# Kernel optimization log

Measured on AMD Instinct MI355X. Metric: run time of the kernel, lower is better.

## Reference

```python
import jax, jax.numpy as jnp
import numpy as np

N_NODES = 200000
N_EDGES = 6400000
IN_CH, HID, OUT_CH = 14, 16, 2


def gcn_conv(x, W, b, src, dst, n_nodes):
    """GCNConv with self-loops and symmetric normalization (PyG defaults).

    out[i] = sum_{j->i} d[i]^-1/2 d[j]^-1/2 (xW)[j] + d[i]^-1 (xW)[i] + b,
    where d = degree(A + I) computed on the target index.
    """
    h = x @ W  # [N, F_out]
    ones = jnp.ones((src.shape[0],), dtype=x.dtype)
    deg = jax.ops.segment_sum(ones, dst, num_segments=n_nodes) + 1.0  # +1 self-loop
    dinv = jax.lax.rsqrt(deg)  # [N]
    norm = dinv[src] * dinv[dst]  # [E]
    msg = h[src] * norm[:, None]  # [E, F_out] -- dominant memory traffic
    agg = jax.ops.segment_sum(msg, dst, num_segments=n_nodes)
    self_loop = h * (dinv * dinv)[:, None]
    return agg + self_loop + b


def setup_inputs() -> dict:
    key = jax.random.key(0)
    k1, k2, k3, k4, k5 = jax.random.split(key, 5)
    x = jax.random.normal(k1, (N_NODES, IN_CH), dtype=jnp.float32)
    edge_index = jax.random.randint(k2, (2, N_EDGES), 0, N_NODES, dtype=jnp.int64)
    edge_attr = jax.random.normal(k3, (N_EDGES, 1), dtype=jnp.float32)  # unused by GCNConv
    s = 1.0 / np.sqrt(IN_CH)
    W1 = jax.random.uniform(k4, (IN_CH, HID), jnp.float32, -s, s)
    b1 = jnp.zeros((HID,), jnp.float32)
    s2 = 1.0 / np.sqrt(HID)
    W2 = jax.random.uniform(k5, (HID, OUT_CH), jnp.float32, -s2, s2)
    b2 = jnp.zeros((OUT_CH,), jnp.float32)
    return {"x": x, "edge_index": edge_index, "edge_attr": edge_attr,
            "W1": W1, "b1": b1, "W2": W2, "b2": b2}


def reference(x, edge_index, edge_attr, W1, b1, W2, b2):
    src, dst = edge_index[0], edge_index[1]
    n = x.shape[0]
    h = jax.nn.relu(gcn_conv(x, W1, b1, src, dst, n))
    # F.dropout(training=self.training) is identity in eval mode
    out = gcn_conv(h, W2, b2, src, dst, n)
    return out
```

## Files before the change

kernel.cpp:

```cpp
#include <hip/hip_runtime.h>
#include <hip/hip_fp16.h>


constexpr int NN = 200000;
constexpr int NE = 6400000;
constexpr int IC = 14;
constexpr int HC = 16;
constexpr int OC = 2;

constexpr int NBK = 392;
constexpr int NSUB = 8;
constexpr int SCAP = 2816;
constexpr int NSEG = NSUB * NBK;
constexpr int CCAP = NSUB * SCAP;
constexpr int SPT = (SCAP + 1023) / 1024;
constexpr int TILE = 5120;
constexpr int BTH = 512;
constexpr int IPT = TILE / BTH;
constexpr int IPT2 = IPT / 2;
constexpr int NTILE = NE / TILE;
constexpr int OVFCAP = 65536;
constexpr int NM = NN / 32;
constexpr int GSTR = 16;

typedef unsigned long long ull;
typedef float f4v __attribute__((ext_vector_type(4)));

__device__ __forceinline__ int phase_of(unsigned src) {
    return src >= 100000u ? (src >= 150000u ? 3 : 2) : (src >= 50000u ? 1 : 0);
}

__device__ __forceinline__ int xcc_id() {
    int x;
    asm volatile("s_getreg_b32 %0, hwreg(HW_REG_XCC_ID)" : "=s"(x));
    return x & 7;
}

__device__ __forceinline__ void acc8(float* av, uint4 u) {
    float2 f0 = __half22float2(*(__half2*)&u.x);
    float2 f1 = __half22float2(*(__half2*)&u.y);
    float2 f2 = __half22float2(*(__half2*)&u.z);
    float2 f3 = __half22float2(*(__half2*)&u.w);
    av[0] += f0.x; av[1] += f0.y; av[2] += f1.x; av[3] += f1.y;
    av[4] += f2.x; av[5] += f2.y; av[6] += f3.x; av[7] += f3.y;
}

__global__ void k_init(int* __restrict__ gcur, const void* __restrict__ ei,
                       int* __restrict__ flag) {
    int i = blockIdx.x * blockDim.x + threadIdx.x;
    if (i < NSEG) gcur[i * GSTR] = i * SCAP;
    else if (i <= NSEG + 4) gcur[i * GSTR] = 0;
    if (i == 500) {
        const ull* p = (const ull*)ei;
        ull acc = 0ULL;
        for (int k = 0; k < 64; ++k) acc |= (p[k] >> 32);
        *flag = (acc == 0ULL) ? 1 : 0;
    }
}

__global__ __launch_bounds__(BTH, 6) void k_binA(const void* __restrict__ ei,
                                                 const int* __restrict__ flag,
                                                 int* __restrict__ gcur,
                                                 unsigned* __restrict__ binned,
                                                 ull* __restrict__ ovf) {
    __shared__ int hist[NBK];
    __shared__ int lofs[NBK];
    __shared__ int gofs[NBK];
    __shared__ int wsum[BTH / 64];
    __shared__ unsigned stage[TILE];

    int t = threadIdx.x;
    int fl = *flag;
    int tile0 = blockIdx.x * TILE;
    int segbase = xcc_id() * NBK;

    if (t < NBK) hist[t] = 0;
    __syncthreads();

    int dbuf[IPT], sbuf[IPT];
    const int* pw = (const int*)ei;
    if (fl) {
#pragma unroll
        for (int k = 0; k < IPT2; ++k) {
            int e = tile0 + k * (2 * BTH) + 2 * t;
            ulonglong2 dd = *(const ulonglong2*)((const long long*)ei + NE + e);
            ulonglong2 ss = *(const ulonglong2*)((const long long*)ei + e);
            dbuf[2 * k] = (int)dd.x;
            dbuf[2 * k + 1] = (int)dd.y;
            sbuf[2 * k] = (int)ss.x;
            sbuf[2 * k + 1] = (int)ss.y;
        }
    } else {
#pragma unroll
        for (int k = 0; k < IPT2; ++k) {
            int e = tile0 + k * (2 * BTH) + 2 * t;
            uint2 dd = *(const uint2*)(pw + NE + e);
            uint2 ss = *(const uint2*)(pw + e);
            dbuf[2 * k] = (int)dd.x;
            dbuf[2 * k + 1] = (int)dd.y;
            sbuf[2 * k] = (int)ss.x;
            sbuf[2 * k + 1] = (int)ss.y;
        }
    }

    unsigned pk[IPT];
    unsigned ra[IPT];
#pragma unroll
    for (int k = 0; k < IPT; ++k) {
        int d = dbuf[k];
        int b = d >> 9;
        int r = atomicAdd(&hist[b], 1);
        pk[k] = ((unsigned)(d & 511) << 18) | (unsigned)sbuf[k];
        ra[k] = ((unsigned)r << 9) | (unsigned)b;
    }
    __syncthreads();

    int h0 = 0, h1 = 0, p = 0;
    if (t < NBK / 2) {
        h0 = hist[2 * t];
        h1 = hist[2 * t + 1];
        p = h0 + h1;
    }
    int lane = t & 63;
    int w = t >> 6;
    int incl = p;
#pragma unroll
    for (int off = 1; off < 64; off <<= 1) {
        int v = __shfl_up(incl, off, 64);
        if (lane >= off) incl += v;
    }
    if (lane == 63) wsum[w] = incl;
    __syncthreads();
    int wbase = 0;
#pragma unroll
    for (int ww = 0; ww < BTH / 64; ++ww) wbase += (ww < w) ? wsum[ww] : 0;
    int ex = wbase + incl - p;
    if (t < NBK / 2) {
        lofs[2 * t] = ex;
        lofs[2 * t + 1] = ex + h0;
    }
    if (t < NBK) gofs[t] = atomicAdd(&gcur[(segbase + t) * GSTR], hist[t]);
    __syncthreads();

#pragma unroll
    for (int k = 0; k < IPT; ++k) {
        int b = (int)(ra[k] & 511u);
        int r = (int)(ra[k] >> 9);
        stage[lofs[b] + r] = pk[k];
    }
    __syncthreads();

    for (int i = t; i < TILE; i += BTH) {
        int b = (i * 313) >> 12;
        if (b > NBK - 1) b = NBK - 1;
        while (b < NBK - 1 && lofs[b + 1] <= i) ++b;
        while (lofs[b] > i) --b;
        unsigned pack = stage[i];
        int seg = segbase + b;
        int dest = gofs[b] + (i - lofs[b]);
        if (dest < (seg + 1) * SCAP) {
            binned[dest] = pack;
        } else {
            int op = atomicAdd(&gcur[NSEG * GSTR], 1);
            if (op < OVFCAP) {
                int d = (b << 9) | (int)(pack >> 18);
                int s = (int)(pack & 0x3FFFF);
                ovf[op] = ((ull)d << 32) | (unsigned)s;
            }
        }
    }
}

__global__ __launch_bounds__(1024, 4) void k_sort(const int* __restrict__ gcur,
                                                  const unsigned* __restrict__ binned,
                                                  const ull* __restrict__ ovf,
                                                  const float* __restrict__ x,
                                                  unsigned* __restrict__ csr,
                                                  float* __restrict__ dinv,
                                                  int* __restrict__ rsg,
                                                  unsigned* __restrict__ spl,
                                                  __half* __restrict__ xph) {
    __shared__ int cnt[2048];
    __shared__ int excl[2048];
    __shared__ int wsum[16];
    __shared__ int nseg[NSUB];
    __shared__ float sdv[512];
    __shared__ unsigned stage[CCAP];
    int b = blockIdx.x;
    int t = threadIdx.x;
    cnt[t] = 0;
    cnt[t + 1024] = 0;
    if (t < NSUB) {
        int seg = t * NBK + b;
        nseg[t] = min(gcur[seg * GSTR] - seg * SCAP, SCAP);
    }
    __syncthreads();
    int nov = min(gcur[NSEG * GSTR], OVFCAP);

    unsigned srcv[NSUB * SPT];
    unsigned rkv[NSUB * SPT];
#pragma unroll
    for (int s = 0; s < NSUB; ++s) {
        int n = nseg[s];
        int sb = (s * NBK + b) * SCAP;
#pragma unroll
        for (int k = 0; k < SPT; ++k) {
            int i = k * 1024 + t;
            rkv[s * SPT + k] = 0xFFFFFFFFu;
            if (i < n) {
                unsigned pack = binned[sb + i];
                unsigned src = pack & 0x3FFFFu;
                int key = ((int)(pack >> 18) << 2) | phase_of(src);
                int r = atomicAdd(&cnt[key], 1);
                srcv[s * SPT + k] = src;
                rkv[s * SPT + k] = ((unsigned)r << 11) | (unsigned)key;
            }
        }
    }
    __syncthreads();

    int h0 = cnt[2 * t];
    int h1 = cnt[2 * t + 1];
    int p = h0 + h1;
    int lane = t & 63;
    int w = t >> 6;
    int incl = p;
#pragma unroll
    for (int off = 1; off < 64; off <<= 1) {
        int v = __shfl_up(incl, off, 64);
        if (lane >= off) incl += v;
    }
    if (lane == 63) wsum[w] = incl;
    __syncthreads();
    int wbase = 0;
#pragma unroll
    for (int ww = 0; ww < 16; ++ww) wbase += (ww < w) ? wsum[ww] : 0;
    int ex = wbase + incl - p;
    excl[2 * t] = ex;
    excl[2 * t + 1] = ex + h0;
    __syncthreads();

#pragma unroll
    for (int c = 0; c < NSUB * SPT; ++c) {
        unsigned rk = rkv[c];
        if (rk != 0xFFFFFFFFu) {
            int key = (int)(rk & 0x7FFu);
            int r = (int)(rk >> 11);
            stage[excl[key] + r] = srcv[c];
        }
    }

    if (t < 512) {
        int g = (b << 9) + t;
        if (g < NN) {
            int c0 = cnt[4 * t];
            int c1 = cnt[4 * t + 1];
            int c2 = cnt[4 * t + 2];
            int c3 = cnt[4 * t + 3];
            int extra = 0;
            for (int k = 0; k < nov; ++k) extra += ((int)(ovf[k] >> 32) == g);
            float dv = rsqrtf((float)(c0 + c1 + c2 + c3 + extra) + 1.0f);
            dinv[g] = dv;
            sdv[t] = dv;
            rsg[g] = b * CCAP + excl[4 * t];
            spl[g] = (unsigned)c0 | ((unsigned)c1 << 8) |
                     ((unsigned)c2 << 16) | ((unsigned)c3 << 24);
        }
    }
    __syncthreads();

    int total = excl[2047] + cnt[2047];
    int tot4 = (total + 3) >> 2;
    const uint4* st4 = (const uint4*)stage;
    uint4* csr4 = (uint4*)(csr + (size_t)b * CCAP);
#pragma unroll
    for (int k = 0; k < (CCAP / 4 + 1023) / 1024; ++k) {
        int i4 = k * 1024 + t;
        if (i4 < tot4) csr4[i4] = st4[i4];
    }

    {
        int n512 = t >> 1;
        int g = (b << 9) + n512;
        if (g < NN) {
            float dv = sdv[n512];
            int cb = 8 * (t & 1);
            const float* xr = x + (size_t)g * IC;
            float v[8];
#pragma unroll
            for (int c = 0; c < 8; c += 2) {
                int ch = cb + c;
                if (ch + 1 < IC) {
                    float2 xx = *(const float2*)(xr + ch);
                    v[c] = dv * xx.x;
                    v[c + 1] = dv * xx.y;
                } else {
                    v[c] = 0.0f;
                    v[c + 1] = 0.0f;
                }
            }
            __half2 p0 = __floats2half2_rn(v[0], v[1]);
            __half2 p1 = __floats2half2_rn(v[2], v[3]);
            __half2 p2 = __floats2half2_rn(v[4], v[5]);
            __half2 p3 = __floats2half2_rn(v[6], v[7]);
            uint4 pk4;
            pk4.x = *(unsigned*)&p0;
            pk4.y = *(unsigned*)&p1;
            pk4.z = *(unsigned*)&p2;
            pk4.w = *(unsigned*)&p3;
            *(uint4*)(xph + (size_t)g * 16 + cb) = pk4;
        }
    }
}

__global__ __launch_bounds__(256) void k_agg1f(const int* __restrict__ rsg,
                                               const unsigned* __restrict__ spl,
                                               const unsigned* __restrict__ csr,
                                               const __half* __restrict__ xph,
                                               const int* __restrict__ gcur,
                                               const ull* __restrict__ ovf,
                                               const float* __restrict__ dinv,
                                               const float* __restrict__ W1,
                                               const float* __restrict__ b1,
                                               const float* __restrict__ W2,
                                               const float* __restrict__ b2,
                                               float2* __restrict__ h2bp,
                                               float2* __restrict__ selfout) {
    __shared__ float sW1[IC * HC];
    __shared__ float sb1[HC];
    __shared__ float sW2[HC * OC];
    __shared__ float sb2[OC];
    __shared__ float sAgg[32][17];
    int t = threadIdx.x;
    if (t < IC * HC) sW1[t] = W1[t];
    if (t < HC) sb1[t] = b1[t];
    if (t < HC * OC) sW2[t] = W2[t];
    if (t < OC) sb2[t] = b2[t];

    int g = t >> 3;
    int h = t & 7;
    int qc = h & 1;
    int eh = h >> 1;
    int i = blockIdx.x * 32 + g;
    unsigned sp = spl[i];
    int tot = (int)(sp & 255u) + (int)((sp >> 8) & 255u) +
              (int)((sp >> 16) & 255u) + (int)(sp >> 24);
    int beg = rsg[i];
    int end = beg + tot;

    float av[8];
#pragma unroll
    for (int c = 0; c < 8; ++c) av[c] = 0.0f;
    int j = beg + eh;
    int s0 = (j < end) ? (int)csr[j] : -1;
    int s1 = (j + 4 < end) ? (int)csr[j + 4] : -1;
    while (j < end) {
        int jn = j + 8;
        int n0 = (jn < end) ? (int)csr[jn] : -1;
        int n1 = (jn + 4 < end) ? (int)csr[jn + 4] : -1;
        uint4 u0 = *(const uint4*)(xph + (size_t)s0 * 16 + 8 * qc);
        acc8(av, u0);
        if (s1 >= 0) {
            uint4 u1 = *(const uint4*)(xph + (size_t)s1 * 16 + 8 * qc);
            acc8(av, u1);
        }
        s0 = n0;
        s1 = n1;
        j = jn;
    }

    if (eh == 0) {
        uint4 us = *(const uint4*)(xph + (size_t)i * 16 + 8 * qc);
        acc8(av, us);
    }
#pragma unroll
    for (int c = 0; c < 8; ++c) av[c] += __shfl_xor(av[c], 2);
#pragma unroll
    for (int c = 0; c < 8; ++c) av[c] += __shfl_xor(av[c], 4);

    float dv = dinv[i];
    if (eh == 0) {
        int nov = min(gcur[NSEG * GSTR], OVFCAP);
        for (int k = 0; k < nov; ++k) {
            ull e = ovf[k];
            if ((int)(e >> 32) == i) {
                int s = (int)(e & 0xFFFFFFFFu);
#pragma unroll
                for (int c = 0; c < 8; ++c)
                    av[c] += __half2float(xph[(size_t)s * 16 + 8 * qc + c]);
            }
        }
#pragma unroll
        for (int c = 0; c < 8; ++c) sAgg[g][8 * qc + c] = dv * av[c];
    }
    __syncthreads();

    int l8 = t & 7;
    float o0 = 0.0f, o1 = 0.0f;
#pragma unroll
    for (int f2 = 0; f2 < 2; ++f2) {
        int f = 2 * l8 + f2;
        float a = sb1[f];
#pragma unroll
        for (int c = 0; c < IC; ++c) a = fmaf(sAgg[g][c], sW1[c * HC + f], a);
        a = fmaxf(a, 0.0f);
        o0 = fmaf(a, sW2[f * OC + 0], o0);
        o1 = fmaf(a, sW2[f * OC + 1], o1);
    }
    o0 += __shfl_xor(o0, 1);
    o1 += __shfl_xor(o1, 1);
    o0 += __shfl_xor(o0, 2);
    o1 += __shfl_xor(o1, 2);
    o0 += __shfl_xor(o0, 4);
    o1 += __shfl_xor(o1, 4);
    if (l8 == 0) {
        h2bp[i] = make_float2(o0 * dv, o1 * dv);
        selfout[i] = make_float2(o0 * dv * dv + sb2[0], o1 * dv * dv + sb2[1]);
    }
}

__global__ __launch_bounds__(256) void k_agg2(const int* __restrict__ rsg,
                                              const unsigned* __restrict__ spl,
                                              const unsigned* __restrict__ csr,
                                              const int* __restrict__ gcur,
                                              const ull* __restrict__ ovf,
                                              const float* __restrict__ dinv,
                                              const float2* __restrict__ h2bp,
                                              const float2* __restrict__ selfout,
                                              float2* __restrict__ out) {
    int tt = blockIdx.x * 256 + threadIdx.x;
    int i = tt >> 3;
    int h = tt & 7;
    if (i >= NN) return;
    unsigned sp = spl[i];
    int tot = (int)(sp & 255u) + (int)((sp >> 8) & 255u) +
              (int)((sp >> 16) & 255u) + (int)(sp >> 24);
    int beg = rsg[i];
    int end = beg + tot;
    float ax = 0.0f, ay = 0.0f;
    int j = beg + h;
    int s0 = (j < end) ? (int)csr[j] : -1;
    int s1 = (j + 8 < end) ? (int)csr[j + 8] : -1;
    while (j < end) {
        int jn = j + 16;
        int n0 = (jn < end) ? (int)csr[jn] : -1;
        int n1 = (jn + 8 < end) ? (int)csr[jn + 8] : -1;
        float2 h0 = h2bp[s0];
        ax += h0.x;
        ay += h0.y;
        if (s1 >= 0) {
            float2 h1 = h2bp[s1];
            ax += h1.x;
            ay += h1.y;
        }
        s0 = n0;
        s1 = n1;
        j = jn;
    }
    ax += __shfl_xor(ax, 1);
    ay += __shfl_xor(ay, 1);
    ax += __shfl_xor(ax, 2);
    ay += __shfl_xor(ay, 2);
    ax += __shfl_xor(ax, 4);
    ay += __shfl_xor(ay, 4);
    if (h == 0) {
        int nov = min(gcur[NSEG * GSTR], OVFCAP);
        for (int k = 0; k < nov; ++k) {
            ull e = ovf[k];
            if ((int)(e >> 32) == i) {
                float2 hh = h2bp[(int)(e & 0xFFFFFFFFu)];
                ax += hh.x;
                ay += hh.y;
            }
        }
        float dv = dinv[i];
        float2 so = selfout[i];
        out[i] = make_float2(so.x + dv * ax, so.y + dv * ay);
    }
}

extern "C" void kernel_launch(void* const* d_in, const int* in_sizes, int n_in,
                              void* d_out, int out_size, void* d_ws, size_t ws_size,
                              hipStream_t stream) {
    const float* x = (const float*)d_in[0];
    const void* ei = d_in[1];
    const float* W1 = (const float*)d_in[3];
    const float* b1 = (const float*)d_in[4];
    const float* W2 = (const float*)d_in[5];
    const float* b2 = (const float*)d_in[6];
    float* out = (float*)d_out;

    ull* ovf = (ull*)d_ws;
    int* gcur = (int*)(ovf + OVFCAP);
    int* flag = gcur + (NSEG + 5) * GSTR;
    int* rsg = flag + 4;
    unsigned* spl = (unsigned*)(rsg + NN);
    float* dinv = (float*)(spl + NN);
    __half* xph = (__half*)(dinv + NN);
    float2* h2bp = (float2*)(xph + (size_t)NN * 16);
    float2* selfout = h2bp + NN;
    unsigned* binned = (unsigned*)(selfout + NN);
    unsigned* csr = binned + (size_t)NSEG * SCAP;

    k_init<<<(NSEG + 5 + 255) / 256, 256, 0, stream>>>(gcur, ei, flag);
    k_binA<<<NTILE, BTH, 0, stream>>>(ei, flag, gcur, binned, ovf);
    k_sort<<<NBK, 1024, 0, stream>>>(gcur, binned, ovf, x, csr, dinv, rsg, spl, xph);
    k_agg1f<<<NM, 256, 0, stream>>>(rsg, spl, csr, xph, gcur, ovf, dinv,
                                    W1, b1, W2, b2, h2bp, selfout);
    k_agg2<<<(NN * 8 + 255) / 256, 256, 0, stream>>>(rsg, spl, csr, gcur, ovf, dinv,
                                                     h2bp, selfout, (float2*)out);
}
```

Measured before the change: 270.3 us.

## Replace CSR sort with direct binned aggregation using shared-memory atomics

Drops the per-bucket counting sort that built a CSR. The two aggregation kernels now stream the binned edge list directly and accumulate into shared-memory float atomics, one block per 256-node bucket. Buckets are halved to 256 nodes (782 per XCC slice) so the per-block accumulators fit in LDS. This removes the sort pass and the CSR write and reread, but it adds heavy LDS atomic contention (16 atomics per edge in layer 1), gives up the src-phase ordering that helped locality of the gathers, and runs only 782 blocks per aggregation kernel.

```diff
diff --git a/kernel.cpp b/kernel.cpp
--- a/kernel.cpp
+++ b/kernel.cpp
@@ -8,27 +8,19 @@
 constexpr int HC = 16;
 constexpr int OC = 2;
 
-constexpr int NBK = 392;
+constexpr int NBK = 782;
 constexpr int NSUB = 8;
-constexpr int SCAP = 2816;
+constexpr int SCAP = 2048;
 constexpr int NSEG = NSUB * NBK;
-constexpr int CCAP = NSUB * SCAP;
-constexpr int SPT = (SCAP + 1023) / 1024;
 constexpr int TILE = 5120;
 constexpr int BTH = 512;
 constexpr int IPT = TILE / BTH;
 constexpr int IPT2 = IPT / 2;
 constexpr int NTILE = NE / TILE;
 constexpr int OVFCAP = 65536;
-constexpr int NM = NN / 32;
 constexpr int GSTR = 16;
 
 typedef unsigned long long ull;
-typedef float f4v __attribute__((ext_vector_type(4)));
-
-__device__ __forceinline__ int phase_of(unsigned src) {
-    return src >= 100000u ? (src >= 150000u ? 3 : 2) : (src >= 50000u ? 1 : 0);
-}
 
 __device__ __forceinline__ int xcc_id() {
     int x;
@@ -36,13 +28,13 @@
     return x & 7;
 }
 
-__device__ __forceinline__ void acc8(float* av, uint4 u) {
+__device__ __forceinline__ void cvt8(float* v, uint4 u) {
     float2 f0 = __half22float2(*(__half2*)&u.x);
     float2 f1 = __half22float2(*(__half2*)&u.y);
     float2 f2 = __half22float2(*(__half2*)&u.z);
     float2 f3 = __half22float2(*(__half2*)&u.w);
-    av[0] += f0.x; av[1] += f0.y; av[2] += f1.x; av[3] += f1.y;
-    av[4] += f2.x; av[5] += f2.y; av[6] += f3.x; av[7] += f3.y;
+    v[0] = f0.x; v[1] = f0.y; v[2] = f1.x; v[3] = f1.y;
+    v[4] = f2.x; v[5] = f2.y; v[6] = f3.x; v[7] = f3.y;
 }
 
 __global__ void k_init(int* __restrict__ gcur, const void* __restrict__ ei,
@@ -75,6 +67,7 @@
     int segbase = xcc_id() * NBK;
 
     if (t < NBK) hist[t] = 0;
+    if (t + BTH < NBK) hist[t + BTH] = 0;
     __syncthreads();
 
     int dbuf[IPT], sbuf[IPT];
@@ -108,10 +101,10 @@
 #pragma unroll
     for (int k = 0; k < IPT; ++k) {
         int d = dbuf[k];
-        int b = d >> 9;
+        int b = d >> 8;
         int r = atomicAdd(&hist[b], 1);
-        pk[k] = ((unsigned)(d & 511) << 18) | (unsigned)sbuf[k];
-        ra[k] = ((unsigned)r << 9) | (unsigned)b;
+        pk[k] = ((unsigned)(d & 255) << 18) | (unsigned)sbuf[k];
+        ra[k] = ((unsigned)r << 10) | (unsigned)b;
     }
     __syncthreads();
 
@@ -140,18 +133,20 @@
         lofs[2 * t + 1] = ex + h0;
     }
     if (t < NBK) gofs[t] = atomicAdd(&gcur[(segbase + t) * GSTR], hist[t]);
+    if (t + BTH < NBK)
+        gofs[t + BTH] = atomicAdd(&gcur[(segbase + t + BTH) * GSTR], hist[t + BTH]);
     __syncthreads();
 
 #pragma unroll
     for (int k = 0; k < IPT; ++k) {
-        int b = (int)(ra[k] & 511u);
-        int r = (int)(ra[k] >> 9);
+        int b = (int)(ra[k] & 1023u);
+        int r = (int)(ra[k] >> 10);
         stage[lofs[b] + r] = pk[k];
     }
     __syncthreads();
 
     for (int i = t; i < TILE; i += BTH) {
-        int b = (i * 313) >> 12;
+        int b = (i * 626) >> 12;
         if (b > NBK - 1) b = NBK - 1;
         while (b < NBK - 1 && lofs[b + 1] <= i) ++b;
         while (lofs[b] > i) --b;
@@ -163,7 +158,7 @@
         } else {
             int op = atomicAdd(&gcur[NSEG * GSTR], 1);
             if (op < OVFCAP) {
-                int d = (b << 9) | (int)(pack >> 18);
+                int d = (b << 8) | (int)(pack >> 18);
                 int s = (int)(pack & 0x3FFFF);
                 ovf[op] = ((ull)d << 32) | (unsigned)s;
             }
@@ -171,25 +166,18 @@
     }
 }
 
-__global__ __launch_bounds__(1024, 4) void k_sort(const int* __restrict__ gcur,
-                                                  const unsigned* __restrict__ binned,
-                                                  const ull* __restrict__ ovf,
-                                                  const float* __restrict__ x,
-                                                  unsigned* __restrict__ csr,
-                                                  float* __restrict__ dinv,
-                                                  int* __restrict__ rsg,
-                                                  unsigned* __restrict__ spl,
-                                                  __half* __restrict__ xph) {
-    __shared__ int cnt[2048];
-    __shared__ int excl[2048];
-    __shared__ int wsum[16];
+__global__ __launch_bounds__(512) void k_degp(const int* __restrict__ gcur,
+                                              const unsigned* __restrict__ binned,
+                                              const ull* __restrict__ ovf,
+                                              const float* __restrict__ x,
+                                              float* __restrict__ dinv,
+                                              __half* __restrict__ xph) {
+    __shared__ int cnt[256];
+    __shared__ float sdv[256];
     __shared__ int nseg[NSUB];
-    __shared__ float sdv[512];
-    __shared__ unsigned stage[CCAP];
     int b = blockIdx.x;
     int t = threadIdx.x;
-    cnt[t] = 0;
-    cnt[t + 1024] = 0;
+    if (t < 256) cnt[t] = 0;
     if (t < NSUB) {
         int seg = t * NBK + b;
         nseg[t] = min(gcur[seg * GSTR] - seg * SCAP, SCAP);
@@ -197,93 +185,33 @@
     __syncthreads();
     int nov = min(gcur[NSEG * GSTR], OVFCAP);
 
-    unsigned srcv[NSUB * SPT];
-    unsigned rkv[NSUB * SPT];
-#pragma unroll
     for (int s = 0; s < NSUB; ++s) {
+        int sb = (s * NBK + b) * SCAP;
         int n = nseg[s];
-        int sb = (s * NBK + b) * SCAP;
-#pragma unroll
-        for (int k = 0; k < SPT; ++k) {
-            int i = k * 1024 + t;
-            rkv[s * SPT + k] = 0xFFFFFFFFu;
-            if (i < n) {
-                unsigned pack = binned[sb + i];
-                unsigned src = pack & 0x3FFFFu;
-                int key = ((int)(pack >> 18) << 2) | phase_of(src);
-                int r = atomicAdd(&cnt[key], 1);
-                srcv[s * SPT + k] = src;
-                rkv[s * SPT + k] = ((unsigned)r << 11) | (unsigned)key;
-            }
-        }
-    }
-    __syncthreads();
-
-    int h0 = cnt[2 * t];
-    int h1 = cnt[2 * t + 1];
-    int p = h0 + h1;
-    int lane = t & 63;
-    int w = t >> 6;
-    int incl = p;
-#pragma unroll
-    for (int off = 1; off < 64; off <<= 1) {
-        int v = __shfl_up(incl, off, 64);
-        if (lane >= off) incl += v;
-    }
-    if (lane == 63) wsum[w] = incl;
-    __syncthreads();
-    int wbase = 0;
-#pragma unroll
-    for (int ww = 0; ww < 16; ++ww) wbase += (ww < w) ? wsum[ww] : 0;
-    int ex = wbase + incl - p;
-    excl[2 * t] = ex;
-    excl[2 * t + 1] = ex + h0;
-    __syncthreads();
-
-#pragma unroll
-    for (int c = 0; c < NSUB * SPT; ++c) {
-        unsigned rk = rkv[c];
-        if (rk != 0xFFFFFFFFu) {
-            int key = (int)(rk & 0x7FFu);
-            int r = (int)(rk >> 11);
-            stage[excl[key] + r] = srcv[c];
-        }
-    }
-
-    if (t < 512) {
-        int g = (b << 9) + t;
+        for (int i = t; i < n; i += 512)
+            atomicAdd(&cnt[binned[sb + i] >> 18], 1);
+    }
+    for (int k = t; k < nov; k += 512) {
+        int d = (int)(ovf[k] >> 32);
+        if ((d >> 8) == b) atomicAdd(&cnt[d & 255], 1);
+    }
+    __syncthreads();
+
+    if (t < 256) {
+        int g = (b << 8) + t;
         if (g < NN) {
-            int c0 = cnt[4 * t];
-            int c1 = cnt[4 * t + 1];
-            int c2 = cnt[4 * t + 2];
-            int c3 = cnt[4 * t + 3];
-            int extra = 0;
-            for (int k = 0; k < nov; ++k) extra += ((int)(ovf[k] >> 32) == g);
-            float dv = rsqrtf((float)(c0 + c1 + c2 + c3 + extra) + 1.0f);
+            float dv = rsqrtf((float)cnt[t] + 1.0f);
             dinv[g] = dv;
             sdv[t] = dv;
-            rsg[g] = b * CCAP + excl[4 * t];
-            spl[g] = (unsigned)c0 | ((unsigned)c1 << 8) |
-                     ((unsigned)c2 << 16) | ((unsigned)c3 << 24);
-        }
-    }
-    __syncthreads();
-
-    int total = excl[2047] + cnt[2047];
-    int tot4 = (total + 3) >> 2;
-    const uint4* st4 = (const uint4*)stage;
-    uint4* csr4 = (uint4*)(csr + (size_t)b * CCAP);
-#pragma unroll
-    for (int k = 0; k < (CCAP / 4 + 1023) / 1024; ++k) {
-        int i4 = k * 1024 + t;
-        if (i4 < tot4) csr4[i4] = st4[i4];
-    }
+        }
+    }
+    __syncthreads();
 
     {
-        int n512 = t >> 1;
-        int g = (b << 9) + n512;
+        int n = t >> 1;
+        int g = (b << 8) + n;
         if (g < NN) {
-            float dv = sdv[n512];
+            float dv = sdv[n];
             int cb = 8 * (t & 1);
             const float* xr = x + (size_t)g * IC;
             float v[8];
@@ -313,12 +241,10 @@
     }
 }
 
-__global__ __launch_bounds__(256) void k_agg1f(const int* __restrict__ rsg,
-                                               const unsigned* __restrict__ spl,
-                                               const unsigned* __restrict__ csr,
+__global__ __launch_bounds__(512) void k_agg1b(const int* __restrict__ gcur,
+                                               const unsigned* __restrict__ binned,
+                                               const ull* __restrict__ ovf,
                                                const __half* __restrict__ xph,
-                                               const int* __restrict__ gcur,
-                                               const ull* __restrict__ ovf,
                                                const float* __restrict__ dinv,
                                                const float* __restrict__ W1,
                                                const float* __restrict__ b1,
@@ -330,152 +256,142 @@
     __shared__ float sb1[HC];
     __shared__ float sW2[HC * OC];
     __shared__ float sb2[OC];
-    __shared__ float sAgg[32][17];
+    __shared__ float acc[256 * 17];
+    __shared__ int nseg[NSUB];
+    int b = blockIdx.x;
     int t = threadIdx.x;
     if (t < IC * HC) sW1[t] = W1[t];
     if (t < HC) sb1[t] = b1[t];
     if (t < HC * OC) sW2[t] = W2[t];
     if (t < OC) sb2[t] = b2[t];
-
-    int g = t >> 3;
-    int h = t & 7;
-    int qc = h & 1;
-    int eh = h >> 1;
-    int i = blockIdx.x * 32 + g;
-    unsigned sp = spl[i];
-    int tot = (int)(sp & 255u) + (int)((sp >> 8) & 255u) +
-              (int)((sp >> 16) & 255u) + (int)(sp >> 24);
-    int beg = rsg[i];
-    int end = beg + tot;
-
-    float av[8];
-#pragma unroll
-    for (int c = 0; c < 8; ++c) av[c] = 0.0f;
-    int j = beg + eh;
-    int s0 = (j < end) ? (int)csr[j] : -1;
-    int s1 = (j + 4 < end) ? (int)csr[j + 4] : -1;
-    while (j < end) {
-        int jn = j + 8;
-        int n0 = (jn < end) ? (int)csr[jn] : -1;
-        int n1 = (jn + 4 < end) ? (int)csr[jn + 4] : -1;
-        uint4 u0 = *(const uint4*)(xph + (size_t)s0 * 16 + 8 * qc);
-        acc8(av, u0);
-        if (s1 >= 0) {
-            uint4 u1 = *(const uint4*)(xph + (size_t)s1 * 16 + 8 * qc);
-            acc8(av, u1);
-        }
-        s0 = n0;
-        s1 = n1;
-        j = jn;
-    }
-
-    if (eh == 0) {
-        uint4 us = *(const uint4*)(xph + (size_t)i * 16 + 8 * qc);
-        acc8(av, us);
-    }
-#pragma unroll
-    for (int c = 0; c < 8; ++c) av[c] += __shfl_xor(av[c], 2);
-#pragma unroll
-    for (int c = 0; c < 8; ++c) av[c] += __shfl_xor(av[c], 4);
-
-    float dv = dinv[i];
-    if (eh == 0) {
-        int nov = min(gcur[NSEG * GSTR], OVFCAP);
-        for (int k = 0; k < nov; ++k) {
-            ull e = ovf[k];
-            if ((int)(e >> 32) == i) {
-                int s = (int)(e & 0xFFFFFFFFu);
-#pragma unroll
-                for (int c = 0; c < 8; ++c)
-                    av[c] += __half2float(xph[(size_t)s * 16 + 8 * qc + c]);
-            }
-        }
-#pragma unroll
-        for (int c = 0; c < 8; ++c) sAgg[g][8 * qc + c] = dv * av[c];
-    }
-    __syncthreads();
-
-    int l8 = t & 7;
+    for (int i = t; i < 256 * 17; i += 512) acc[i] = 0.0f;
+    if (t < NSUB) {
+        int seg = t * NBK + b;
+        nseg[t] = min(gcur[seg * GSTR] - seg * SCAP, SCAP);
+    }
+    __syncthreads();
+    int nov = min(gcur[NSEG * GSTR], OVFCAP);
+
+    for (int s = 0; s < NSUB; ++s) {
+        int sb = (s * NBK + b) * SCAP;
+        int n = nseg[s];
+        for (int i = t; i < n; i += 512) {
+            unsigned pack = binned[sb + i];
+            int dlow = (int)(pack >> 18);
+            unsigned src = pack & 0x3FFFFu;
+            uint4 u0 = *(const uint4*)(xph + (size_t)src * 16);
+            uint4 u1 = *(const uint4*)(xph + (size_t)src * 16 + 8);
+            float v[16];
+            cvt8(v, u0);
+            cvt8(v + 8, u1);
+            int base = dlow * 17;
+#pragma unroll
+            for (int c = 0; c < 16; ++c) atomicAdd(&acc[base + c], v[c]);
+        }
+    }
+    for (int k = t; k < nov; k += 512) {
+        ull e = ovf[k];
+        int d = (int)(e >> 32);
+        if ((d >> 8) == b) {
+            unsigned src = (unsigned)(e & 0xFFFFFFFFu);
+            uint4 u0 = *(const uint4*)(xph + (size_t)src * 16);
+            uint4 u1 = *(const uint4*)(xph + (size_t)src * 16 + 8);
+            float v[16];
+            cvt8(v, u0);
+            cvt8(v + 8, u1);
+            int base = (d & 255) * 17;
+#pragma unroll
+            for (int c = 0; c < 16; ++c) atomicAdd(&acc[base + c], v[c]);
+        }
+    }
+    __syncthreads();
+
+    int n = t >> 1;
+    int hf = t & 1;
+    int g = (b << 8) + n;
+    float dv = 0.0f;
+    if (g < NN) {
+        dv = dinv[g];
+        uint4 us = *(const uint4*)(xph + (size_t)g * 16 + 8 * hf);
+        float sv[8];
+        cvt8(sv, us);
+#pragma unroll
+        for (int c = 0; c < 8; ++c) {
+            int a = n * 17 + 8 * hf + c;
+            acc[a] = (acc[a] + sv[c]) * dv;
+        }
+    }
+    __syncthreads();
+
     float o0 = 0.0f, o1 = 0.0f;
-#pragma unroll
-    for (int f2 = 0; f2 < 2; ++f2) {
-        int f = 2 * l8 + f2;
-        float a = sb1[f];
-#pragma unroll
-        for (int c = 0; c < IC; ++c) a = fmaf(sAgg[g][c], sW1[c * HC + f], a);
-        a = fmaxf(a, 0.0f);
-        o0 = fmaf(a, sW2[f * OC + 0], o0);
-        o1 = fmaf(a, sW2[f * OC + 1], o1);
+    if (g < NN) {
+#pragma unroll
+        for (int f8 = 0; f8 < 8; ++f8) {
+            int f = hf * 8 + f8;
+            float a = sb1[f];
+#pragma unroll
+            for (int c = 0; c < IC; ++c) a = fmaf(acc[n * 17 + c], sW1[c * HC + f], a);
+            a = fmaxf(a, 0.0f);
+            o0 = fmaf(a, sW2[f * OC + 0], o0);
+            o1 = fmaf(a, sW2[f * OC + 1], o1);
+        }
     }
     o0 += __shfl_xor(o0, 1);
     o1 += __shfl_xor(o1, 1);
-    o0 += __shfl_xor(o0, 2);
-    o1 += __shfl_xor(o1, 2);
-    o0 += __shfl_xor(o0, 4);
-    o1 += __shfl_xor(o1, 4);
-    if (l8 == 0) {
-        h2bp[i] = make_float2(o0 * dv, o1 * dv);
-        selfout[i] = make_float2(o0 * dv * dv + sb2[0], o1 * dv * dv + sb2[1]);
-    }
-}
-
-__global__ __launch_bounds__(256) void k_agg2(const int* __restrict__ rsg,
-                                              const unsigned* __restrict__ spl,
-                                              const unsigned* __restrict__ csr,
-                                              const int* __restrict__ gcur,
-                                              const ull* __restrict__ ovf,
-                                              const float* __restrict__ dinv,
-                                              const float2* __restrict__ h2bp,
-                                              const float2* __restrict__ selfout,
-                                              float2* __restrict__ out) {
-    int tt = blockIdx.x * 256 + threadIdx.x;
-    int i = tt >> 3;
-    int h = tt & 7;
-    if (i >= NN) return;
-    unsigned sp = spl[i];
-    int tot = (int)(sp & 255u) + (int)((sp >> 8) & 255u) +
-              (int)((sp >> 16) & 255u) + (int)(sp >> 24);
-    int beg = rsg[i];
-    int end = beg + tot;
-    float ax = 0.0f, ay = 0.0f;
-    int j = beg + h;
-    int s0 = (j < end) ? (int)csr[j] : -1;
-    int s1 = (j + 8 < end) ? (int)csr[j + 8] : -1;
-    while (j < end) {
-        int jn = j + 16;
-        int n0 = (jn < end) ? (int)csr[jn] : -1;
-        int n1 = (jn + 8 < end) ? (int)csr[jn + 8] : -1;
-        float2 h0 = h2bp[s0];
-        ax += h0.x;
-        ay += h0.y;
-        if (s1 >= 0) {
-            float2 h1 = h2bp[s1];
-            ax += h1.x;
-            ay += h1.y;
-        }
-        s0 = n0;
-        s1 = n1;
-        j = jn;
-    }
-    ax += __shfl_xor(ax, 1);
-    ay += __shfl_xor(ay, 1);
-    ax += __shfl_xor(ax, 2);
-    ay += __shfl_xor(ay, 2);
-    ax += __shfl_xor(ax, 4);
-    ay += __shfl_xor(ay, 4);
-    if (h == 0) {
-        int nov = min(gcur[NSEG * GSTR], OVFCAP);
-        for (int k = 0; k < nov; ++k) {
-            ull e = ovf[k];
-            if ((int)(e >> 32) == i) {
-                float2 hh = h2bp[(int)(e & 0xFFFFFFFFu)];
-                ax += hh.x;
-                ay += hh.y;
-            }
-        }
-        float dv = dinv[i];
-        float2 so = selfout[i];
-        out[i] = make_float2(so.x + dv * ax, so.y + dv * ay);
+    if (g < NN && hf == 0) {
+        h2bp[g] = make_float2(o0 * dv, o1 * dv);
+        selfout[g] = make_float2(o0 * dv * dv + sb2[0], o1 * dv * dv + sb2[1]);
+    }
+}
+
+__global__ __launch_bounds__(512) void k_agg2b(const int* __restrict__ gcur,
+                                               const unsigned* __restrict__ binned,
+                                               const ull* __restrict__ ovf,
+                                               const float2* __restrict__ h2bp,
+                                               const float2* __restrict__ selfout,
+                                               const float* __restrict__ dinv,
+                                               float2* __restrict__ out) {
+    __shared__ float acc2[512];
+    __shared__ int nseg[NSUB];
+    int b = blockIdx.x;
+    int t = threadIdx.x;
+    acc2[t] = 0.0f;
+    if (t < NSUB) {
+        int seg = t * NBK + b;
+        nseg[t] = min(gcur[seg * GSTR] - seg * SCAP, SCAP);
+    }
+    __syncthreads();
+    int nov = min(gcur[NSEG * GSTR], OVFCAP);
+
+    for (int s = 0; s < NSUB; ++s) {
+        int sb = (s * NBK + b) * SCAP;
+        int n = nseg[s];
+        for (int i = t; i < n; i += 512) {
+            unsigned pack = binned[sb + i];
+            int dlow = (int)(pack >> 18);
+            float2 hv = h2bp[pack & 0x3FFFFu];
+            atomicAdd(&acc2[2 * dlow], hv.x);
+            atomicAdd(&acc2[2 * dlow + 1], hv.y);
+        }
+    }
+    for (int k = t; k < nov; k += 512) {
+        ull e = ovf[k];
+        int d = (int)(e >> 32);
+        if ((d >> 8) == b) {
+            float2 hv = h2bp[(unsigned)(e & 0xFFFFFFFFu)];
+            atomicAdd(&acc2[2 * (d & 255)], hv.x);
+            atomicAdd(&acc2[2 * (d & 255) + 1], hv.y);
+        }
+    }
+    __syncthreads();
+
+    if (t < 256) {
+        int g = (b << 8) + t;
+        if (g < NN) {
+            float dv = dinv[g];
+            float2 so = selfout[g];
+            out[g] = make_float2(so.x + dv * acc2[2 * t], so.y + dv * acc2[2 * t + 1]);
+        }
     }
 }
 
@@ -493,20 +409,17 @@
     ull* ovf = (ull*)d_ws;
     int* gcur = (int*)(ovf + OVFCAP);
     int* flag = gcur + (NSEG + 5) * GSTR;
-    int* rsg = flag + 4;
-    unsigned* spl = (unsigned*)(rsg + NN);
-    float* dinv = (float*)(spl + NN);
+    float* dinv = (float*)(flag + 4);
     __half* xph = (__half*)(dinv + NN);
     float2* h2bp = (float2*)(xph + (size_t)NN * 16);
     float2* selfout = h2bp + NN;
     unsigned* binned = (unsigned*)(selfout + NN);
-    unsigned* csr = binned + (size_t)NSEG * SCAP;
 
     k_init<<<(NSEG + 5 + 255) / 256, 256, 0, stream>>>(gcur, ei, flag);
     k_binA<<<NTILE, BTH, 0, stream>>>(ei, flag, gcur, binned, ovf);
-    k_sort<<<NBK, 1024, 0, stream>>>(gcur, binned, ovf, x, csr, dinv, rsg, spl, xph);
-    k_agg1f<<<NM, 256, 0, stream>>>(rsg, spl, csr, xph, gcur, ovf, dinv,
-                                    W1, b1, W2, b2, h2bp, selfout);
-    k_agg2<<<(NN * 8 + 255) / 256, 256, 0, stream>>>(rsg, spl, csr, gcur, ovf, dinv,
-                                                     h2bp, selfout, (float2*)out);
-}
+    k_degp<<<NBK, 512, 0, stream>>>(gcur, binned, ovf, x, dinv, xph);
+    k_agg1b<<<NBK, 512, 0, stream>>>(gcur, binned, ovf, xph, dinv,
+                                     W1, b1, W2, b2, h2bp, selfout);
+    k_agg2b<<<NBK, 512, 0, stream>>>(gcur, binned, ovf, h2bp, selfout, dinv,
+                                     (float2*)out);
+}
```

Result: slower. 931.0 us (+244.4%).
